# Performance work log

Measured on AMD Instinct MI355X. Metric: run time of the kernel, lower is better.

The kernel has to match this reference:

```python
import jax, jax.numpy as jnp
import numpy as np

N = 100000          # nodes
E = 1600000         # random edges (self loops appended in reference)
F_IN = 256          # dataset.num_features
NUM_CLASSES = 7     # dataset.num_classes
H = 2 * NUM_CLASSES # heads = 14
C = NUM_CLASSES     # per-head channels (concat=False)
NEG_SLOPE = 0.2     # GATConv default leaky_relu slope


def setup_inputs() -> dict:
    key = jax.random.key(0)
    ks = jax.random.split(key, 10)
    x = jax.random.normal(ks[0], (N, F_IN), jnp.float32)
    edge_index = jax.random.randint(ks[1], (2, E), 0, N, jnp.int32)
    def glorot(k, shape, fan_in):
        return jax.random.normal(k, shape, jnp.float32) * (1.0 / np.sqrt(fan_in))
    return {
        "x": x,
        "edge_index": edge_index,
        "W1": glorot(ks[2], (F_IN, H * C), F_IN),
        "a_src1": glorot(ks[3], (H, C), C),
        "a_dst1": glorot(ks[4], (H, C), C),
        "b1": jnp.zeros((C,), jnp.float32),
        "W2": glorot(ks[5], (C, H * C), C),
        "a_src2": glorot(ks[6], (H, C), C),
        "a_dst2": glorot(ks[7], (H, C), C),
        "b2": jnp.zeros((C,), jnp.float32),
    }


def gat_conv(x, src, dst, W, a_src, a_dst, b):
    # x: [N, Fin] -> per-head projections [N, H, C]
    xh = (x @ W).reshape(N, H, C)
    # per-node attention logits [N, H]
    al_src = jnp.einsum("nhc,hc->nh", xh, a_src)
    al_dst = jnp.einsum("nhc,hc->nh", xh, a_dst)
    # per-edge logits (message flows src -> dst)
    alpha = jax.nn.leaky_relu(al_src[src] + al_dst[dst], NEG_SLOPE)  # [E', H]
    # segment softmax over incoming edges of each destination node
    amax = jax.ops.segment_max(jax.lax.stop_gradient(alpha), dst, num_segments=N)
    alpha = jnp.exp(alpha - amax[dst])
    denom = jax.ops.segment_sum(alpha, dst, num_segments=N)
    alpha = alpha / denom[dst]
    # weighted messages, then MAX aggregation per destination (aggr='max')
    msg = alpha[:, :, None] * xh[src]                    # [E', H, C]
    out = jax.ops.segment_max(msg, dst, num_segments=N)  # [N, H, C]
    # concat=False -> mean over heads, plus bias
    return out.mean(axis=1) + b                          # [N, C]


def reference(x, edge_index, W1, a_src1, a_dst1, b1, W2, a_src2, a_dst2, b2):
    # GATConv(add_self_loops=True): append self loops so every node has >=1 in-edge
    loops = jnp.arange(N, dtype=edge_index.dtype)
    src = jnp.concatenate([edge_index[0], loops])
    dst = jnp.concatenate([edge_index[1], loops])
    h = gat_conv(x, src, dst, W1, a_src1, a_dst1, b1)
    h = jax.nn.relu(h)
    h = gat_conv(h, src, dst, W2, a_src2, a_dst2, b2)
    return jax.nn.log_softmax(h, axis=1)
```

## Files before the change

### kernel.cpp

```cpp
#include <hip/hip_runtime.h>
#include <math.h>

#define H  14
#define C  7
#define HC 98
#define FIN 256
#define NEG_SLOPE 0.2f
#define NPB 32
#define AGG_BLOCK (NPB * H)

#define BSHIFT 7
#define BSIZE  128
#define NBUCK_MAX 1024

typedef __attribute__((ext_vector_type(8))) short short8;
typedef __attribute__((ext_vector_type(4))) float floatx4;

#define WT_ROWS   112
#define WT_STRIDE 264
#define XA_STRIDE 40

__device__ __forceinline__ unsigned bf16r(float f) {
    unsigned u = __float_as_uint(f);
    return (u + 0x7FFFu + ((u >> 16) & 1u)) >> 16;
}
__device__ __forceinline__ float bflo(unsigned w) { return __uint_as_float(w << 16); }
__device__ __forceinline__ float bfhi(unsigned w) { return __uint_as_float(w & 0xFFFF0000u); }


__global__ void k_zero(int* __restrict__ p, int n) {
    int i = blockIdx.x * blockDim.x + threadIdx.x;
    if (i < n) p[i] = 0;
}

__global__ __launch_bounds__(256) void k_hist(const int* __restrict__ ei, int E,
                                              int* __restrict__ gcnt, int nb) {
    __shared__ int hist[NBUCK_MAX];
    const int t = threadIdx.x;
    for (int i = t; i < nb; i += 256) hist[i] = 0;
    __syncthreads();
    const int stride = gridDim.x * 256;
    for (int e = blockIdx.x * 256 + t; e < E; e += stride)
        atomicAdd(&hist[ei[E + e] >> BSHIFT], 1);
    __syncthreads();
    for (int i = t; i < nb; i += 256)
        if (hist[i]) atomicAdd(gcnt + i, hist[i]);
}

__global__ __launch_bounds__(1024) void k_bscan(const int* __restrict__ gcnt,
                                                int* __restrict__ boff, int* __restrict__ bcur,
                                                int* __restrict__ row_ptr, int nb, int N) {
    __shared__ int sd[1024];
    int t = threadIdx.x;
    int own = (t < nb) ? gcnt[t] : 0;
    sd[t] = own;
    __syncthreads();
    #pragma unroll
    for (int off = 1; off < 1024; off <<= 1) {
        int v = (t >= off) ? sd[t - off] : 0;
        __syncthreads();
        sd[t] += v;
        __syncthreads();
    }
    if (t < nb) {
        boff[t + 1] = sd[t];
        bcur[t] = sd[t] - own;
        if (t == nb - 1) row_ptr[N] = sd[t];
    }
    if (t == 0) boff[0] = 0;
}

__global__ __launch_bounds__(256) void k_part(const int* __restrict__ ei, int E,
                                              int* __restrict__ bcur, int2* __restrict__ pedge,
                                              int nb) {
    __shared__ int hist[NBUCK_MAX];
    __shared__ int start[NBUCK_MAX];
    const int t = threadIdx.x;
    const int chunk = (E + gridDim.x - 1) / gridDim.x;
    const int c0 = blockIdx.x * chunk;
    const int c1 = min(c0 + chunk, E);
    for (int i = t; i < nb; i += 256) hist[i] = 0;
    __syncthreads();
    for (int e = c0 + t; e < c1; e += 256)
        atomicAdd(&hist[ei[E + e] >> BSHIFT], 1);
    __syncthreads();
    for (int i = t; i < nb; i += 256) {
        int h = hist[i];
        start[i] = h ? atomicAdd(bcur + i, h) : 0;
        hist[i] = 0;
    }
    __syncthreads();
    for (int e = c0 + t; e < c1; e += 256) {
        int s = ei[e], d = ei[E + e];
        int b = d >> BSHIFT;
        int pos = start[b] + atomicAdd(&hist[b], 1);
        pedge[pos] = make_int2(s, d);
    }
}

__global__ __launch_bounds__(256) void k_bcsr(const int2* __restrict__ pedge,
                                              const int* __restrict__ boff,
                                              int* __restrict__ row_ptr, int* __restrict__ col,
                                              int N) {
    __shared__ int cnt[BSIZE];
    __shared__ int sc[BSIZE];
    __shared__ int cur[BSIZE];
    const int b  = blockIdx.x;
    const int t  = threadIdx.x;
    const int e0 = boff[b], e1 = boff[b + 1];
    const int base = b << BSHIFT;
    const int nv = min(BSIZE, N - base);
    if (t < BSIZE) cnt[t] = 0;
    __syncthreads();
    for (int e = e0 + t; e < e1; e += 256)
        atomicAdd(&cnt[pedge[e].y - base], 1);
    __syncthreads();
    if (t < BSIZE) sc[t] = cnt[t];
    __syncthreads();
    #pragma unroll
    for (int off = 1; off < BSIZE; off <<= 1) {
        int v = 0;
        if (t < BSIZE && t >= off) v = sc[t - off];
        __syncthreads();
        if (t < BSIZE) sc[t] += v;
        __syncthreads();
    }
    if (t < nv) {
        int excl = sc[t] - cnt[t];
        row_ptr[base + t] = e0 + excl;
        cur[t] = excl;
    }
    __syncthreads();
    for (int e = e0 + t; e < e1; e += 256) {
        int2 r = pedge[e];
        int d = r.y - base;
        int pos = e0 + atomicAdd(&cur[d], 1);
        col[pos] = r.x;
    }
}


__global__ void k_convW(const float* __restrict__ W, unsigned short* __restrict__ WtG) {
    int id = blockIdx.x * blockDim.x + threadIdx.x;
    int n = id >> 8, k = id & 255;
    float v = (n < HC) ? W[k * HC + n] : 0.f;
    WtG[id] = (unsigned short)(__float_as_uint(v) >> 16);
}

__global__ __launch_bounds__(256) void k_proj1_mfma(
    const float* __restrict__ x, const unsigned short* __restrict__ WtG,
    unsigned short* __restrict__ xhb, int N)
{
    __shared__ unsigned short wt_s[WT_ROWS * WT_STRIDE];
    __shared__ unsigned short xa_s[64 * XA_STRIDE];
    const int t  = threadIdx.x;
    const int wv = t >> 6;
    const int l  = t & 63;
    const int ln = l & 15;
    const int qd = l >> 4;
    const int rowBase = blockIdx.x * 64;

    #pragma unroll
    for (int i = 0; i < 14; ++i) {
        int f = i * 256 + t;
        int r = f >> 5, pos = f & 31;
        *(uint4*)(wt_s + r * WT_STRIDE + pos * 8) = ((const uint4*)WtG)[f];
    }

    floatx4 acc[7] = {};

    for (int step = 0; step < 8; ++step) {
        const int k0 = step * 32;
        __syncthreads();
        #pragma unroll
        for (int i = 0; i < 2; ++i) {
            int idx = i * 256 + t;
            int r = idx >> 3, c4 = idx & 7;
            int gr = rowBase + r; if (gr >= N) gr = N - 1;
            float4 v = *(const float4*)(x + (size_t)gr * FIN + k0 + c4 * 4);
            ushort4 u;
            u.x = (unsigned short)(__float_as_uint(v.x) >> 16);
            u.y = (unsigned short)(__float_as_uint(v.y) >> 16);
            u.z = (unsigned short)(__float_as_uint(v.z) >> 16);
            u.w = (unsigned short)(__float_as_uint(v.w) >> 16);
            *(ushort4*)(xa_s + r * XA_STRIDE + c4 * 4) = u;
        }
        __syncthreads();
        short8 a = *(const short8*)(xa_s + ((wv << 4) + ln) * XA_STRIDE + qd * 8);
        #pragma unroll
        for (int ct = 0; ct < 7; ++ct) {
            short8 b = *(const short8*)(wt_s + (ct * 16 + ln) * WT_STRIDE + k0 + qd * 8);
            acc[ct] = __builtin_amdgcn_mfma_f32_16x16x32_bf16(a, b, acc[ct], 0, 0, 0);
        }
    }

    #pragma unroll
    for (int ct = 0; ct < 7; ++ct) {
        #pragma unroll
        for (int r = 0; r < 4; ++r) {
            int gr   = rowBase + (wv << 4) + (qd << 2) + r;
            int colg = ct * 16 + ln;
            if (gr < N && colg < HC)
                xhb[(size_t)gr * HC + colg] = (unsigned short)bf16r(acc[ct][r]);
        }
    }
}

__global__ void k_pack1(const unsigned short* __restrict__ xhb,
                        const float* __restrict__ asrc, const float* __restrict__ adst,
                        uint4* __restrict__ xpack, float* __restrict__ aldst, int NH)
{
    int id = blockIdx.x * blockDim.x + threadIdx.x;
    if (id >= NH) return;
    int n = id / H, h = id - n * H;
    const unsigned short* xp = xhb + (size_t)n * HC + h * C;
    unsigned v[C];
    float s1 = 0.f, s2 = 0.f;
    #pragma unroll
    for (int c2 = 0; c2 < C; ++c2) {
        v[c2] = xp[c2];
        float f = bflo(v[c2]);
        s1 = fmaf(f, asrc[h * C + c2], s1);
        s2 = fmaf(f, adst[h * C + c2], s2);
    }
    uint4 pk;
    pk.x = v[0] | (v[1] << 16);
    pk.y = v[2] | (v[3] << 16);
    pk.z = v[4] | (v[5] << 16);
    pk.w = v[6] | (bf16r(s1) << 16);
    xpack[id] = pk;
    aldst[id] = s2;
}


__global__ __launch_bounds__(256) void k_proj2_pack(
    const float* __restrict__ h1, const float* __restrict__ W,
    const float* __restrict__ asrc, const float* __restrict__ adst,
    uint4* __restrict__ xpack, float* __restrict__ aldst, int N)
{
    __shared__ float Ws[C * HC];
    __shared__ float as_s[HC], ad_s[HC];
    const int t = threadIdx.x;
    for (int i = t; i < C * HC; i += 256) Ws[i] = W[i];
    if (t < HC) { as_s[t] = asrc[t]; ad_s[t] = adst[t]; }
    __syncthreads();
    int n = blockIdx.x * 256 + t;
    if (n >= N) return;
    float xr[C];
    #pragma unroll
    for (int c2 = 0; c2 < C; ++c2) xr[c2] = h1[(size_t)n * C + c2];
    #pragma unroll
    for (int h = 0; h < H; ++h) {
        float v[C], s1 = 0.f, s2 = 0.f;
        #pragma unroll
        for (int c2 = 0; c2 < C; ++c2) {
            float acc = 0.f;
            #pragma unroll
            for (int k = 0; k < C; ++k)
                acc = fmaf(xr[k], Ws[k * HC + h * C + c2], acc);
            v[c2] = acc;
            s1 = fmaf(acc, as_s[h * C + c2], s1);
            s2 = fmaf(acc, ad_s[h * C + c2], s2);
        }
        uint4 pk;
        pk.x = bf16r(v[0]) | (bf16r(v[1]) << 16);
        pk.y = bf16r(v[2]) | (bf16r(v[3]) << 16);
        pk.z = bf16r(v[4]) | (bf16r(v[5]) << 16);
        pk.w = bf16r(v[6]) | (bf16r(s1) << 16);
        xpack[(size_t)n * H + h] = pk;
        aldst[(size_t)n * H + h] = s2;
    }
}


template<int LAYER>
__global__ __launch_bounds__(AGG_BLOCK) void k_agg(
    const int* __restrict__ row_ptr, const int* __restrict__ col,
    const uint4* __restrict__ xpack, const float* __restrict__ aldst,
    const float* __restrict__ bias,
    float* __restrict__ h1, float* __restrict__ out, int N)
{
    __shared__ float vals[NPB][HC];
    __shared__ float fv[NPB][C];
    const int t  = threadIdx.x;
    const int nl = t / H;
    const int h  = t - nl * H;
    const int n  = blockIdx.x * NPB + nl;

    if (n < N) {
        const int e0  = row_ptr[n];
        const int deg = row_ptr[n + 1] - e0;
        const float ld = aldst[(size_t)n * H + h];
        float m, den, mx[C];
        {
            uint4 pk = xpack[(size_t)n * H + h];
            float l = bfhi(pk.w) + ld;
            l = (l > 0.f) ? l : NEG_SLOPE * l;
            m = l; den = 1.f;
            mx[0] = bflo(pk.x); mx[1] = bfhi(pk.x);
            mx[2] = bflo(pk.y); mx[3] = bfhi(pk.y);
            mx[4] = bflo(pk.z); mx[5] = bfhi(pk.z);
            mx[6] = bflo(pk.w);
        }
        uint4 pkN;
        if (deg > 0) pkN = xpack[(size_t)col[e0] * H + h];
        for (int i = 0; i < deg; ++i) {
            uint4 cur = pkN;
            if (i + 1 < deg) pkN = xpack[(size_t)col[e0 + i + 1] * H + h];
            float l = bfhi(cur.w) + ld;
            l = (l > 0.f) ? l : NEG_SLOPE * l;
            float mn = fmaxf(m, l);
            float r  = __expf(m - mn);
            float p  = __expf(l - mn);
            den = den * r + p;
            mx[0] = fmaxf(mx[0] * r, p * bflo(cur.x));
            mx[1] = fmaxf(mx[1] * r, p * bfhi(cur.x));
            mx[2] = fmaxf(mx[2] * r, p * bflo(cur.y));
            mx[3] = fmaxf(mx[3] * r, p * bfhi(cur.y));
            mx[4] = fmaxf(mx[4] * r, p * bflo(cur.z));
            mx[5] = fmaxf(mx[5] * r, p * bfhi(cur.z));
            mx[6] = fmaxf(mx[6] * r, p * bflo(cur.w));
            m = mn;
        }
        float rd = 1.f / den;
        #pragma unroll
        for (int c2 = 0; c2 < C; ++c2) vals[nl][h * C + c2] = mx[c2] * rd;
    }
    __syncthreads();

    if (t < NPB * C) {
        int nl2 = t / C, c2 = t - nl2 * C;
        int n2 = blockIdx.x * NPB + nl2;
        if (n2 < N) {
            float s = 0.f;
            #pragma unroll
            for (int hh = 0; hh < H; ++hh) s += vals[nl2][hh * C + c2];
            float o = s * (1.f / H) + bias[c2];
            if (LAYER == 1) h1[(size_t)n2 * C + c2] = fmaxf(o, 0.f);
            else            fv[nl2][c2] = o;
        }
    }
    if (LAYER == 2) {
        __syncthreads();
        if (t < NPB) {
            int n2 = blockIdx.x * NPB + t;
            if (n2 < N) {
                float mv = -1e30f;
                #pragma unroll
                for (int c2 = 0; c2 < C; ++c2) mv = fmaxf(mv, fv[t][c2]);
                float lse = 0.f;
                #pragma unroll
                for (int c2 = 0; c2 < C; ++c2) lse += __expf(fv[t][c2] - mv);
                lse = logf(lse);
                #pragma unroll
                for (int c2 = 0; c2 < C; ++c2)
                    out[(size_t)n2 * C + c2] = fv[t][c2] - mv - lse;
            }
        }
    }
}


static inline size_t align16(size_t v) { return (v + 15) & ~(size_t)15; }

extern "C" void kernel_launch(void* const* d_in, const int* in_sizes, int n_in,
                              void* d_out, int out_size, void* d_ws, size_t ws_size,
                              hipStream_t stream)
{
    const float* x     = (const float*)d_in[0];
    const int*   ei    = (const int*)d_in[1];
    const float* W1    = (const float*)d_in[2];
    const float* asrc1 = (const float*)d_in[3];
    const float* adst1 = (const float*)d_in[4];
    const float* b1    = (const float*)d_in[5];
    const float* W2    = (const float*)d_in[6];
    const float* asrc2 = (const float*)d_in[7];
    const float* adst2 = (const float*)d_in[8];
    const float* b2    = (const float*)d_in[9];

    const int N  = in_sizes[0] / FIN;
    const int E  = in_sizes[1] / 2;
    const int nb = (N + BSIZE - 1) >> BSHIFT;

    char* w = (char*)d_ws;
    uint4* xpack   = (uint4*)w; w += align16((size_t)N * H * 16);
    char*  shared  = w;         w += align16((size_t)E * 8 > (size_t)N * HC * 2
                                             ? (size_t)E * 8 : (size_t)N * HC * 2);
    int2*  pedge   = (int2*)shared;
    unsigned short* xhb = (unsigned short*)shared;
    float* aldst   = (float*)w; w += align16((size_t)N * H * 4);
    float* h1      = (float*)w; w += align16((size_t)N * C * 4);
    int*   row_ptr = (int*)w;   w += align16((size_t)(N + 1) * 4);
    int*   col     = (int*)w;   w += align16((size_t)E * 4);
    int*   gcnt    = (int*)w;   w += align16((size_t)nb * 4);
    int*   boff    = (int*)w;   w += align16((size_t)(nb + 1) * 4);
    int*   bcur    = (int*)w;   w += align16((size_t)nb * 4);
    unsigned short* WtG = (unsigned short*)w; w += align16((size_t)WT_ROWS * FIN * 2);

    const int gAgg  = (N + NPB - 1) / NPB;
    const int gMfma = (N + 63) / 64;
    const int gNH   = (N * H + 255) / 256;
    const int g256N = (N + 255) / 256;

    k_zero<<<(nb + 255) / 256, 256, 0, stream>>>(gcnt, nb);
    k_hist<<<256, 256, 0, stream>>>(ei, E, gcnt, nb);
    k_bscan<<<1, 1024, 0, stream>>>(gcnt, boff, bcur, row_ptr, nb, N);
    k_part<<<256, 256, 0, stream>>>(ei, E, bcur, pedge, nb);
    k_bcsr<<<nb, 256, 0, stream>>>(pedge, boff, row_ptr, col, N);

    k_convW<<<(WT_ROWS * FIN + 255) / 256, 256, 0, stream>>>(W1, WtG);
    k_proj1_mfma<<<gMfma, 256, 0, stream>>>(x, WtG, xhb, N);
    k_pack1<<<gNH, 256, 0, stream>>>(xhb, asrc1, adst1, xpack, aldst, N * H);
    k_agg<1><<<gAgg, AGG_BLOCK, 0, stream>>>(row_ptr, col, xpack, aldst, b1,
                                             h1, (float*)d_out, N);
    k_proj2_pack<<<g256N, 256, 0, stream>>>(h1, W2, asrc2, adst2, xpack, aldst, N);
    k_agg<2><<<gAgg, AGG_BLOCK, 0, stream>>>(row_ptr, col, xpack, aldst, b2,
                                             h1, (float*)d_out, N);
}
```

Before: 473.8 us.

## Fuse pack into MFMA projection, deepen agg prefetch, enlarge CSR buckets

Folds the attention-logit and bf16 packing step into the MFMA projection kernel by staging the accumulators in reused shared memory. This removes the intermediate xhb buffer round-trip and one launch. The aggregation loop now prefetches four neighbor rows ahead instead of one to hide gather latency, at the cost of extra registers. CSR bucket size grows from 128 to 512 nodes with 512-thread blocks, giving fewer buckets and fewer blocks but more shared-memory atomic contention per block.

```diff
diff --git a/kernel.cpp b/kernel.cpp
--- a/kernel.cpp
+++ b/kernel.cpp
@@ -9,9 +9,9 @@
 #define NPB 32
 #define AGG_BLOCK (NPB * H)
 
-#define BSHIFT 7
-#define BSIZE  128
-#define NBUCK_MAX 1024
+#define BSHIFT 9
+#define BSIZE  512
+#define NBUCK_MAX 256
 
 typedef __attribute__((ext_vector_type(8))) short short8;
 typedef __attribute__((ext_vector_type(4))) float floatx4;
@@ -19,6 +19,7 @@
 #define WT_ROWS   112
 #define WT_STRIDE 264
 #define XA_STRIDE 40
+#define VS_STRIDE 99
 
 __device__ __forceinline__ unsigned bf16r(float f) {
     unsigned u = __float_as_uint(f);
@@ -98,7 +99,7 @@
     }
 }
 
-__global__ __launch_bounds__(256) void k_bcsr(const int2* __restrict__ pedge,
+__global__ __launch_bounds__(512) void k_bcsr(const int2* __restrict__ pedge,
                                               const int* __restrict__ boff,
                                               int* __restrict__ row_ptr, int* __restrict__ col,
                                               int N) {
@@ -110,19 +111,18 @@
     const int e0 = boff[b], e1 = boff[b + 1];
     const int base = b << BSHIFT;
     const int nv = min(BSIZE, N - base);
-    if (t < BSIZE) cnt[t] = 0;
-    __syncthreads();
-    for (int e = e0 + t; e < e1; e += 256)
+    cnt[t] = 0;
+    __syncthreads();
+    for (int e = e0 + t; e < e1; e += 512)
         atomicAdd(&cnt[pedge[e].y - base], 1);
     __syncthreads();
-    if (t < BSIZE) sc[t] = cnt[t];
+    sc[t] = cnt[t];
     __syncthreads();
     #pragma unroll
     for (int off = 1; off < BSIZE; off <<= 1) {
-        int v = 0;
-        if (t < BSIZE && t >= off) v = sc[t - off];
-        __syncthreads();
-        if (t < BSIZE) sc[t] += v;
+        int v = (t >= off) ? sc[t - off] : 0;
+        __syncthreads();
+        sc[t] += v;
         __syncthreads();
     }
     if (t < nv) {
@@ -131,7 +131,7 @@
         cur[t] = excl;
     }
     __syncthreads();
-    for (int e = e0 + t; e < e1; e += 256) {
+    for (int e = e0 + t; e < e1; e += 512) {
         int2 r = pedge[e];
         int d = r.y - base;
         int pos = e0 + atomicAdd(&cur[d], 1);
@@ -149,10 +149,13 @@
 
 __global__ __launch_bounds__(256) void k_proj1_mfma(
     const float* __restrict__ x, const unsigned short* __restrict__ WtG,
-    unsigned short* __restrict__ xhb, int N)
+    const float* __restrict__ asrc, const float* __restrict__ adst,
+    uint4* __restrict__ xpack, float* __restrict__ aldst, int N)
 {
     __shared__ unsigned short wt_s[WT_ROWS * WT_STRIDE];
     __shared__ unsigned short xa_s[64 * XA_STRIDE];
+    __shared__ float as_s[HC], ad_s[HC];
+    float* vals_s = (float*)wt_s;
     const int t  = threadIdx.x;
     const int wv = t >> 6;
     const int l  = t & 63;
@@ -166,6 +169,7 @@
         int r = f >> 5, pos = f & 31;
         *(uint4*)(wt_s + r * WT_STRIDE + pos * 8) = ((const uint4*)WtG)[f];
     }
+    if (t < HC) { as_s[t] = asrc[t]; ad_s[t] = adst[t]; }
 
     floatx4 acc[7] = {};
 
@@ -194,42 +198,40 @@
         }
     }
 
+    __syncthreads();
     #pragma unroll
     for (int ct = 0; ct < 7; ++ct) {
+        int colg = ct * 16 + ln;
+        if (colg < HC) {
+            #pragma unroll
+            for (int r = 0; r < 4; ++r)
+                vals_s[((wv << 4) + (qd << 2) + r) * VS_STRIDE + colg] = acc[ct][r];
+        }
+    }
+    __syncthreads();
+
+    for (int p = t; p < 64 * H; p += 256) {
+        int nl = p / H, h = p - nl * H;
+        int gn = rowBase + nl;
+        if (gn >= N) break;
+        const float* vp = vals_s + nl * VS_STRIDE + h * C;
+        unsigned v[C];
+        float s1 = 0.f, s2 = 0.f;
         #pragma unroll
-        for (int r = 0; r < 4; ++r) {
-            int gr   = rowBase + (wv << 4) + (qd << 2) + r;
-            int colg = ct * 16 + ln;
-            if (gr < N && colg < HC)
-                xhb[(size_t)gr * HC + colg] = (unsigned short)bf16r(acc[ct][r]);
-        }
-    }
-}
-
-__global__ void k_pack1(const unsigned short* __restrict__ xhb,
-                        const float* __restrict__ asrc, const float* __restrict__ adst,
-                        uint4* __restrict__ xpack, float* __restrict__ aldst, int NH)
-{
-    int id = blockIdx.x * blockDim.x + threadIdx.x;
-    if (id >= NH) return;
-    int n = id / H, h = id - n * H;
-    const unsigned short* xp = xhb + (size_t)n * HC + h * C;
-    unsigned v[C];
-    float s1 = 0.f, s2 = 0.f;
-    #pragma unroll
-    for (int c2 = 0; c2 < C; ++c2) {
-        v[c2] = xp[c2];
-        float f = bflo(v[c2]);
-        s1 = fmaf(f, asrc[h * C + c2], s1);
-        s2 = fmaf(f, adst[h * C + c2], s2);
-    }
-    uint4 pk;
-    pk.x = v[0] | (v[1] << 16);
-    pk.y = v[2] | (v[3] << 16);
-    pk.z = v[4] | (v[5] << 16);
-    pk.w = v[6] | (bf16r(s1) << 16);
-    xpack[id] = pk;
-    aldst[id] = s2;
+        for (int c2 = 0; c2 < C; ++c2) {
+            float f = vp[c2];
+            v[c2] = bf16r(f);
+            s1 = fmaf(f, as_s[h * C + c2], s1);
+            s2 = fmaf(f, ad_s[h * C + c2], s2);
+        }
+        uint4 pk;
+        pk.x = v[0] | (v[1] << 16);
+        pk.y = v[2] | (v[3] << 16);
+        pk.z = v[4] | (v[5] << 16);
+        pk.w = v[6] | (bf16r(s1) << 16);
+        xpack[(size_t)gn * H + h] = pk;
+        aldst[(size_t)gn * H + h] = s2;
+    }
 }
 
 
@@ -302,25 +304,31 @@
             mx[4] = bflo(pk.z); mx[5] = bfhi(pk.z);
             mx[6] = bflo(pk.w);
         }
-        uint4 pkN;
-        if (deg > 0) pkN = xpack[(size_t)col[e0] * H + h];
-        for (int i = 0; i < deg; ++i) {
-            uint4 cur = pkN;
-            if (i + 1 < deg) pkN = xpack[(size_t)col[e0 + i + 1] * H + h];
-            float l = bfhi(cur.w) + ld;
-            l = (l > 0.f) ? l : NEG_SLOPE * l;
-            float mn = fmaxf(m, l);
-            float r  = __expf(m - mn);
-            float p  = __expf(l - mn);
-            den = den * r + p;
-            mx[0] = fmaxf(mx[0] * r, p * bflo(cur.x));
-            mx[1] = fmaxf(mx[1] * r, p * bfhi(cur.x));
-            mx[2] = fmaxf(mx[2] * r, p * bflo(cur.y));
-            mx[3] = fmaxf(mx[3] * r, p * bfhi(cur.y));
-            mx[4] = fmaxf(mx[4] * r, p * bflo(cur.z));
-            mx[5] = fmaxf(mx[5] * r, p * bfhi(cur.z));
-            mx[6] = fmaxf(mx[6] * r, p * bflo(cur.w));
-            m = mn;
+        if (deg > 0) {
+            const int last = deg - 1;
+            uint4 b0 = xpack[(size_t)col[e0] * H + h];
+            uint4 b1 = xpack[(size_t)col[e0 + min(1, last)] * H + h];
+            uint4 b2 = xpack[(size_t)col[e0 + min(2, last)] * H + h];
+            uint4 b3 = xpack[(size_t)col[e0 + min(3, last)] * H + h];
+            for (int i = 0; i < deg; ++i) {
+                uint4 cur = b0;
+                b0 = b1; b1 = b2; b2 = b3;
+                b3 = xpack[(size_t)col[e0 + min(i + 4, last)] * H + h];
+                float l = bfhi(cur.w) + ld;
+                l = (l > 0.f) ? l : NEG_SLOPE * l;
+                float mn = fmaxf(m, l);
+                float r  = __expf(m - mn);
+                float p  = __expf(l - mn);
+                den = den * r + p;
+                mx[0] = fmaxf(mx[0] * r, p * bflo(cur.x));
+                mx[1] = fmaxf(mx[1] * r, p * bfhi(cur.x));
+                mx[2] = fmaxf(mx[2] * r, p * bflo(cur.y));
+                mx[3] = fmaxf(mx[3] * r, p * bfhi(cur.y));
+                mx[4] = fmaxf(mx[4] * r, p * bflo(cur.z));
+                mx[5] = fmaxf(mx[5] * r, p * bfhi(cur.z));
+                mx[6] = fmaxf(mx[6] * r, p * bflo(cur.w));
+                m = mn;
+            }
         }
         float rd = 1.f / den;
         #pragma unroll
@@ -384,10 +392,7 @@
 
     char* w = (char*)d_ws;
     uint4* xpack   = (uint4*)w; w += align16((size_t)N * H * 16);
-    char*  shared  = w;         w += align16((size_t)E * 8 > (size_t)N * HC * 2
-                                             ? (size_t)E * 8 : (size_t)N * HC * 2);
-    int2*  pedge   = (int2*)shared;
-    unsigned short* xhb = (unsigned short*)shared;
+    int2*  pedge   = (int2*)w;  w += align16((size_t)E * 8);
     float* aldst   = (float*)w; w += align16((size_t)N * H * 4);
     float* h1      = (float*)w; w += align16((size_t)N * C * 4);
     int*   row_ptr = (int*)w;   w += align16((size_t)(N + 1) * 4);
@@ -399,18 +404,16 @@
 
     const int gAgg  = (N + NPB - 1) / NPB;
     const int gMfma = (N + 63) / 64;
-    const int gNH   = (N * H + 255) / 256;
     const int g256N = (N + 255) / 256;
 
-    k_zero<<<(nb + 255) / 256, 256, 0, stream>>>(gcnt, nb);
+    k_zero<<<1, 256, 0, stream>>>(gcnt, nb);
     k_hist<<<256, 256, 0, stream>>>(ei, E, gcnt, nb);
     k_bscan<<<1, 1024, 0, stream>>>(gcnt, boff, bcur, row_ptr, nb, N);
     k_part<<<256, 256, 0, stream>>>(ei, E, bcur, pedge, nb);
-    k_bcsr<<<nb, 256, 0, stream>>>(pedge, boff, row_ptr, col, N);
+    k_bcsr<<<nb, 512, 0, stream>>>(pedge, boff, row_ptr, col, N);
 
     k_convW<<<(WT_ROWS * FIN + 255) / 256, 256, 0, stream>>>(W1, WtG);
-    k_proj1_mfma<<<gMfma, 256, 0, stream>>>(x, WtG, xhb, N);
-    k_pack1<<<gNH, 256, 0, stream>>>(xhb, asrc1, adst1, xpack, aldst, N * H);
+    k_proj1_mfma<<<gMfma, 256, 0, stream>>>(x, WtG, asrc1, adst1, xpack, aldst, N);
     k_agg<1><<<gAgg, AGG_BLOCK, 0, stream>>>(row_ptr, col, xpack, aldst, b1,
                                              h1, (float*)d_out, N);
     k_proj2_pack<<<g256N, 256, 0, stream>>>(h1, W2, asrc2, adst2, xpack, aldst, N);
```

Measured after the change: 479.3 us. About the same (+1.1%).
